# Performance work log

Hardware: AMD Instinct MI355X
Metric: run time of the kernel (lower is better)

Reference implementation:

```python
import jax, jax.numpy as jnp
import numpy as np

B, S, T, D = 64, 256, 8, 256
E, M = 500000, 2048
NEG_INF = -10000000000.0


def setup_inputs() -> dict:
    key = jax.random.key(0)
    ks = jax.random.split(key, 9)
    token_reprs = jax.random.normal(ks[0], (B, S, T, D), dtype=jnp.float32)
    w1 = jax.random.normal(ks[1], (D, D // 2), dtype=jnp.float32) * (1.0 / np.sqrt(D))
    b1 = jnp.zeros((D // 2,), dtype=jnp.float32)
    w2 = jax.random.normal(ks[2], (D // 2, 1), dtype=jnp.float32) * (1.0 / np.sqrt(D // 2))
    b2 = jnp.zeros((1,), dtype=jnp.float32)
    edge_index = jax.random.randint(ks[3], (2, E), 0, B * S, dtype=jnp.int32)
    lm_indices = jax.random.randint(ks[4], (M,), 0, B * S * T, dtype=jnp.int32)
    batch_pointers = jax.random.randint(ks[5], (M,), 0, B, dtype=jnp.int32)
    tree_padding_mask = jax.random.randint(ks[6], (B, S), 0, 2, dtype=jnp.int32).astype(jnp.bool_)
    return {
        "token_reprs": token_reprs,
        "w1": w1, "b1": b1, "w2": w2, "b2": b2,
        "edge_index": edge_index,
        "lm_indices": lm_indices,
        "batch_pointers": batch_pointers,
        "tree_padding_mask": tree_padding_mask,
    }


def reference(token_reprs, w1, b1, w2, b2, edge_index, lm_indices, batch_pointers, tree_padding_mask):
    b, s, t, d = token_reprs.shape
    # type representation is the first token of each type tree
    type_reprs = token_reprs[:, :, 0]                  # [B, S, D]
    flat_types = type_reprs.reshape(b * s, d)          # [B*S, D]

    # predict_lemmas: gather scope/goal reprs, elementwise multiply, 2-layer MLP
    scope_ids, goal_ids = edge_index[0], edge_index[1]
    h = flat_types[scope_ids] * flat_types[goal_ids]   # [E, D]
    h = h @ w1 + b1                                    # [E, D//2] (Dropout is identity in eval)
    lemmas = (h @ w2 + b2)[:, 0]                       # [E]

    # predict_masks: gather masked token reprs + per-tree candidates, dot, mask
    mask_reprs = token_reprs.reshape(b * s * t, d)[lm_indices]  # [M, D]
    candidates = type_reprs[batch_pointers]            # [M, S, D]
    candidate_mask = tree_padding_mask[batch_pointers] # [M, S]
    lm_preds = jnp.einsum('md,msd->ms', mask_reprs, candidates)
    lm_preds = jnp.where(candidate_mask, lm_preds, NEG_INF)
    return lemmas, lm_preds
```

## Files before the change

kernel.cpp:

```cpp
#include <hip/hip_runtime.h>

#define DD 256
#define SS 256
#define BB 64
#define NEDGE 500000
#define MM 2048
#define NEG_INF -10000000000.0f
#define ROWF4 512
#define NROWS (BB * SS)
#define EBLK 1954

#define OFF_VC     0
#define OFF_MSORT  2048
#define OFF_BSTART 10240
#define OFF_HIST   16384
#define OFF_EPAIR  (1 << 20)
#define OFF_EORIG  (6 << 20)
#define OFF_P2     (8 << 20)
#define OFF_QROW   (16 << 20)
#define OFF_MROWS  (24 << 20)

typedef _Float16 h2 __attribute__((ext_vector_type(2)));

__device__ __forceinline__ h2 uh(unsigned u) {
    union { unsigned x; h2 h; } c; c.x = u; return c.h;
}
__device__ __forceinline__ unsigned hpack(float a, float b) {
    union { h2 h; unsigned u; } c;
    c.h = h2{(_Float16)a, (_Float16)b};
    return c.u;
}

#if __has_builtin(__builtin_amdgcn_fdot2)
__device__ __forceinline__ float FDOT2(h2 a, h2 b, float c) {
    return __builtin_amdgcn_fdot2(a, b, c, false);
}
#else
__device__ __forceinline__ float FDOT2(h2 a, h2 b, float c) {
    return c + (float)a.x * (float)b.x + (float)a.y * (float)b.y;
}
#endif

__device__ __forceinline__ float dot16(uint4 a, uint4 b, float acc) {
    acc = FDOT2(uh(a.x), uh(b.x), acc);
    acc = FDOT2(uh(a.y), uh(b.y), acc);
    acc = FDOT2(uh(a.z), uh(b.z), acc);
    acc = FDOT2(uh(a.w), uh(b.w), acc);
    return acc;
}

__global__ void setup_k(const float* __restrict__ w1, const float* __restrict__ b1,
                        const float* __restrict__ w2, const float* __restrict__ b2,
                        const int* __restrict__ bp,
                        float* __restrict__ vc, int* __restrict__ msorted,
                        int* __restrict__ bstart, int* __restrict__ hist) {
    const int t = threadIdx.x;
    if (blockIdx.x == 0) {
        float acc = 0.f;
        #pragma unroll 4
        for (int j = 0; j < DD / 2; ++j) acc += w1[t * (DD / 2) + j] * w2[j];
        vc[t] = acc;
        if (t == 0) {
            float c = b2[0];
            for (int j = 0; j < DD / 2; ++j) c += b1[j] * w2[j];
            vc[DD] = c;
        }
    } else if (blockIdx.x == 1) {
        __shared__ int h[BB];
        __shared__ int offs[BB + 1];
        if (t < BB) h[t] = 0;
        __syncthreads();
        for (int m = t; m < MM; m += 256) atomicAdd(&h[bp[m]], 1);
        __syncthreads();
        if (t == 0) {
            int acc = 0;
            for (int i = 0; i < BB; ++i) { offs[i] = acc; acc += h[i]; }
            offs[BB] = acc;
        }
        __syncthreads();
        if (t < BB + 1) bstart[t] = offs[t];
        __syncthreads();
        for (int m = t; m < MM; m += 256) {
            int pos = atomicAdd(&offs[bp[m]], 1);
            msorted[pos] = m;
        }
    } else {
        for (int f = t; f < NROWS; f += 256) hist[f] = 0;
    }
}

__global__ __launch_bounds__(256) void compact_hist(
        const float* __restrict__ tok, const int* __restrict__ lmi,
        const int* __restrict__ edges, const float* __restrict__ vc,
        unsigned* __restrict__ p2u, unsigned* __restrict__ qrow,
        unsigned* __restrict__ mru, int* __restrict__ hist) {
    const int t = threadIdx.x;
    const int lane = t & 63, w = t >> 6;
    const int bid = blockIdx.x;
    if (bid < NROWS / 4) {
        const int row = bid * 4 + w;
        const float4 a = ((const float4*)tok)[(size_t)row * ROWF4 + lane];
        const float4 v = ((const float4*)vc)[lane];
        ((uint2*)p2u)[(size_t)row * 64 + lane] =
            make_uint2(hpack(a.x, a.y), hpack(a.z, a.w));
        ((uint2*)qrow)[(size_t)row * 64 + lane] =
            make_uint2(hpack(a.x * v.x, a.y * v.y), hpack(a.z * v.z, a.w * v.w));
    } else if (bid < NROWS / 4 + MM / 4) {
        const int m = (bid - NROWS / 4) * 4 + w;
        const float4 a = ((const float4*)(tok + (size_t)lmi[m] * DD))[lane];
        ((uint2*)mru)[(size_t)m * 64 + lane] =
            make_uint2(hpack(a.x, a.y), hpack(a.z, a.w));
    } else {
        const int e = (bid - NROWS / 4 - MM / 4) * 256 + t;
        if (e < NEDGE) atomicAdd(&hist[__builtin_nontemporal_load(edges + e)], 1);
    }
}

__global__ __launch_bounds__(256) void prefix_k(int* __restrict__ hist) {
    __shared__ int loc[NROWS];
    __shared__ int part[256];
    __shared__ int scan[256];
    const int t = threadIdx.x;
    for (int f = t; f < NROWS; f += 256) loc[f] = hist[f];
    __syncthreads();
    int s = 0;
    for (int j = 0; j < 64; ++j) s += loc[t * 64 + j];
    part[t] = s;
    __syncthreads();
    if (t == 0) {
        int a = 0;
        for (int i = 0; i < 256; ++i) { scan[i] = a; a += part[i]; }
    }
    __syncthreads();
    int a = scan[t];
    for (int j = 0; j < 64; ++j) {
        int c = loc[t * 64 + j];
        loc[t * 64 + j] = a;
        a += c;
    }
    __syncthreads();
    for (int f = t; f < NROWS; f += 256) hist[f] = loc[f];
}

__global__ __launch_bounds__(256) void scatter_k(
        const int* __restrict__ edges, int* __restrict__ hist,
        uint2* __restrict__ epair, unsigned* __restrict__ eorig) {
    const int e = blockIdx.x * 256 + threadIdx.x;
    if (e >= NEDGE) return;
    const int sc = __builtin_nontemporal_load(edges + e);
    const int gl = __builtin_nontemporal_load(edges + NEDGE + e);
    const int pos = atomicAdd(&hist[sc], 1);
    epair[pos] = make_uint2((unsigned)sc, (unsigned)gl);
    eorig[pos] = (unsigned)e;
}

__global__ __launch_bounds__(256) void edge_sorted(
        const unsigned* __restrict__ qrow, const unsigned* __restrict__ p2u,
        const uint2* __restrict__ epair, const unsigned* __restrict__ eorig,
        const float* __restrict__ vc, float* __restrict__ out) {
    const int t = threadIdx.x;
    const int l32 = t & 31, grp = t >> 5;
    __shared__ uint2 sPair[256];
    __shared__ unsigned sOrig[256];
    __shared__ float sRes[256];
    const int idx = blockIdx.x * 256 + t;
    const bool val = idx < NEDGE;
    sPair[t] = val ? epair[idx] : make_uint2(0u, 0u);
    sOrig[t] = val ? eorig[idx] : 0u;
    const float c = vc[DD];
    __syncthreads();

    const uint4* Q = (const uint4*)qrow;
    const uint4* A = (const uint4*)p2u;
    #pragma unroll 2
    for (int ii = 0; ii < 32; ++ii) {
        const int slot = grp * 32 + ii;
        const uint2 pr = sPair[slot];
        const uint4 qa = Q[(size_t)pr.x * 32 + l32];
        const uint4 ab = A[(size_t)pr.y * 32 + l32];
        float r = dot16(qa, ab, 0.f);
        r += __shfl_down(r, 16, 32);
        r += __shfl_down(r, 8, 32);
        r += __shfl_down(r, 4, 32);
        r += __shfl_down(r, 2, 32);
        r += __shfl_down(r, 1, 32);
        if (l32 == 0) sRes[slot] = r + c;
    }
    __syncthreads();
    if (val) __builtin_nontemporal_store(sRes[t], out + sOrig[t]);
}

__global__ __launch_bounds__(256) void lm_gemm(
        const unsigned* __restrict__ p2u,
        const unsigned* __restrict__ mru,
        const int* __restrict__ msorted,
        const int* __restrict__ bstart,
        const int* __restrict__ tpm,
        float* __restrict__ out) {
    const int b  = blockIdx.x;
    const int st = blockIdx.y;
    const int ch = blockIdx.z;
    const int s0 = bstart[b], nmt = bstart[b + 1] - s0;
    const int base = ch * 32;
    if (base >= nmt) return;
    const int nm = min(32, nmt - base);
    const int t = threadIdx.x;

    __shared__ uint4 candS[64 * 33];
    __shared__ uint4 maskS[32 * 33];
    __shared__ int mids[32];

    if (t < 32) mids[t] = msorted[s0 + base + min(t, nm - 1)];
    __syncthreads();
    for (int f = t; f < 32 * 32; f += 256) {
        const int r = f >> 5, q = f & 31;
        maskS[r * 33 + q] = ((const uint4*)mru)[(size_t)mids[r] * 32 + q];
    }
    for (int f = t; f < 64 * 32; f += 256) {
        const int r = f >> 5, q = f & 31;
        candS[r * 33 + q] = ((const uint4*)p2u)[((size_t)b * SS + st * 64 + r) * 32 + q];
    }
    __syncthreads();

    const int tmg = t & 15, tsg = t >> 4;
    float acc[2][4];
    #pragma unroll
    for (int im = 0; im < 2; ++im)
        #pragma unroll
        for (int ss = 0; ss < 4; ++ss) acc[im][ss] = 0.f;

    #pragma unroll 4
    for (int j = 0; j < 32; ++j) {
        const uint4 a0 = maskS[tmg * 33 + j];
        const uint4 a1 = maskS[(tmg + 16) * 33 + j];
        #pragma unroll
        for (int ss = 0; ss < 4; ++ss) {
            const uint4 bb = candS[(tsg * 4 + ss) * 33 + j];
            acc[0][ss] = dot16(a0, bb, acc[0][ss]);
            acc[1][ss] = dot16(a1, bb, acc[1][ss]);
        }
    }

    const int col0 = st * 64 + tsg * 4;
    float4 msk;
    msk.x = tpm[b * SS + col0] ? 1.f : 0.f;
    msk.y = tpm[b * SS + col0 + 1] ? 1.f : 0.f;
    msk.z = tpm[b * SS + col0 + 2] ? 1.f : 0.f;
    msk.w = tpm[b * SS + col0 + 3] ? 1.f : 0.f;
    #pragma unroll
    for (int im = 0; im < 2; ++im) {
        const int mi = tmg + im * 16;
        if (mi < nm) {
            float4 o;
            o.x = msk.x != 0.f ? acc[im][0] : NEG_INF;
            o.y = msk.y != 0.f ? acc[im][1] : NEG_INF;
            o.z = msk.z != 0.f ? acc[im][2] : NEG_INF;
            o.w = msk.w != 0.f ? acc[im][3] : NEG_INF;
            *(float4*)&out[(size_t)mids[mi] * SS + col0] = o;
        }
    }
}

extern "C" void kernel_launch(void* const* d_in, const int* in_sizes, int n_in,
                              void* d_out, int out_size, void* d_ws, size_t ws_size,
                              hipStream_t stream) {
    const float* tok = (const float*)d_in[0];
    const float* w1  = (const float*)d_in[1];
    const float* b1  = (const float*)d_in[2];
    const float* w2  = (const float*)d_in[3];
    const float* b2  = (const float*)d_in[4];
    const int* edges = (const int*)d_in[5];
    const int* lmi   = (const int*)d_in[6];
    const int* bp    = (const int*)d_in[7];
    const int* tpm   = (const int*)d_in[8];

    float* out_lemmas = (float*)d_out;
    float* out_lm     = (float*)d_out + NEDGE;

    char* ws = (char*)d_ws;
    float* vc       = (float*)(ws + OFF_VC);
    int* msorted    = (int*)(ws + OFF_MSORT);
    int* bstart     = (int*)(ws + OFF_BSTART);
    int* hist       = (int*)(ws + OFF_HIST);
    uint2* epair    = (uint2*)(ws + OFF_EPAIR);
    unsigned* eorig = (unsigned*)(ws + OFF_EORIG);
    unsigned* p2u   = (unsigned*)(ws + OFF_P2);
    unsigned* qrow  = (unsigned*)(ws + OFF_QROW);
    unsigned* mru   = (unsigned*)(ws + OFF_MROWS);

    setup_k<<<3, 256, 0, stream>>>(w1, b1, w2, b2, bp, vc, msorted, bstart, hist);
    compact_hist<<<NROWS / 4 + MM / 4 + EBLK, 256, 0, stream>>>(
        tok, lmi, edges, vc, p2u, qrow, mru, hist);
    prefix_k<<<1, 256, 0, stream>>>(hist);
    scatter_k<<<EBLK, 256, 0, stream>>>(edges, hist, epair, eorig);
    edge_sorted<<<EBLK, 256, 0, stream>>>(qrow, p2u, epair, eorig, vc, out_lemmas);
    lm_gemm<<<dim3(BB, 4, 4), 256, 0, stream>>>(p2u, mru, msorted, bstart, tpm, out_lm);
}
```

Baseline: 297.4 us.

## Bucket edges by scope/goal row ranges and pin buckets to XCDs

Replaces the full counting sort of edges by scope row (16K-bin histogram plus a single-block prefix scan) with a coarse 64-bucket sort keyed on the high bits of scope and goal ids. Each block builds a shared-memory histogram first, which cuts global atomics. The edge kernel now launches 512 persistent blocks, each handling an eighth of its assigned buckets, with blockIdx mod 8 steering its bucket sequence so each XCD's L2 works on one row range at a time. It writes results directly to out[eorig] and drops the staged shared-memory gather. The trade-off is a looser scope ordering, uncoalesced scattered stores, and load imbalance within a bucket.

```diff
diff --git a/kernel.cpp b/kernel.cpp
--- a/kernel.cpp
+++ b/kernel.cpp
@@ -13,7 +13,8 @@
 #define OFF_VC     0
 #define OFF_MSORT  2048
 #define OFF_BSTART 10240
-#define OFF_HIST   16384
+#define OFF_EBKT   11264
+#define OFF_CURS   12288
 #define OFF_EPAIR  (1 << 20)
 #define OFF_EORIG  (6 << 20)
 #define OFF_P2     (8 << 20)
@@ -53,7 +54,8 @@
                         const float* __restrict__ w2, const float* __restrict__ b2,
                         const int* __restrict__ bp,
                         float* __restrict__ vc, int* __restrict__ msorted,
-                        int* __restrict__ bstart, int* __restrict__ hist) {
+                        int* __restrict__ bstart, int* __restrict__ ebkt,
+                        int* __restrict__ cursor) {
     const int t = threadIdx.x;
     if (blockIdx.x == 0) {
         float acc = 0.f;
@@ -85,7 +87,8 @@
             msorted[pos] = m;
         }
     } else {
-        for (int f = t; f < NROWS; f += 256) hist[f] = 0;
+        if (t < 65) ebkt[t] = 0;
+        if (t < 64) cursor[t] = 0;
     }
 }
 
@@ -93,7 +96,7 @@
         const float* __restrict__ tok, const int* __restrict__ lmi,
         const int* __restrict__ edges, const float* __restrict__ vc,
         unsigned* __restrict__ p2u, unsigned* __restrict__ qrow,
-        unsigned* __restrict__ mru, int* __restrict__ hist) {
+        unsigned* __restrict__ mru, int* __restrict__ ebkt) {
     const int t = threadIdx.x;
     const int lane = t & 63, w = t >> 6;
     const int bid = blockIdx.x;
@@ -111,83 +114,94 @@
         ((uint2*)mru)[(size_t)m * 64 + lane] =
             make_uint2(hpack(a.x, a.y), hpack(a.z, a.w));
     } else {
+        __shared__ int lh[64];
+        if (t < 64) lh[t] = 0;
+        __syncthreads();
         const int e = (bid - NROWS / 4 - MM / 4) * 256 + t;
-        if (e < NEDGE) atomicAdd(&hist[__builtin_nontemporal_load(edges + e)], 1);
-    }
-}
-
-__global__ __launch_bounds__(256) void prefix_k(int* __restrict__ hist) {
-    __shared__ int loc[NROWS];
-    __shared__ int part[256];
-    __shared__ int scan[256];
-    const int t = threadIdx.x;
-    for (int f = t; f < NROWS; f += 256) loc[f] = hist[f];
-    __syncthreads();
-    int s = 0;
-    for (int j = 0; j < 64; ++j) s += loc[t * 64 + j];
-    part[t] = s;
-    __syncthreads();
-    if (t == 0) {
-        int a = 0;
-        for (int i = 0; i < 256; ++i) { scan[i] = a; a += part[i]; }
-    }
-    __syncthreads();
-    int a = scan[t];
-    for (int j = 0; j < 64; ++j) {
-        int c = loc[t * 64 + j];
-        loc[t * 64 + j] = a;
-        a += c;
-    }
-    __syncthreads();
-    for (int f = t; f < NROWS; f += 256) hist[f] = loc[f];
+        if (e < NEDGE) {
+            const int sc = __builtin_nontemporal_load(edges + e);
+            const int gl = __builtin_nontemporal_load(edges + NEDGE + e);
+            atomicAdd(&lh[(sc >> 11) * 8 + (gl >> 11)], 1);
+        }
+        __syncthreads();
+        if (t < 64 && lh[t]) atomicAdd(&ebkt[t], lh[t]);
+    }
+}
+
+__global__ void prefix64(int* __restrict__ ebkt, int* __restrict__ cursor) {
+    if (threadIdx.x == 0) {
+        int acc = 0;
+        for (int i = 0; i < 64; ++i) {
+            int c = ebkt[i];
+            ebkt[i] = acc; cursor[i] = acc;
+            acc += c;
+        }
+        ebkt[64] = acc;
+    }
 }
 
 __global__ __launch_bounds__(256) void scatter_k(
-        const int* __restrict__ edges, int* __restrict__ hist,
+        const int* __restrict__ edges, int* __restrict__ cursor,
         uint2* __restrict__ epair, unsigned* __restrict__ eorig) {
-    const int e = blockIdx.x * 256 + threadIdx.x;
-    if (e >= NEDGE) return;
-    const int sc = __builtin_nontemporal_load(edges + e);
-    const int gl = __builtin_nontemporal_load(edges + NEDGE + e);
-    const int pos = atomicAdd(&hist[sc], 1);
-    epair[pos] = make_uint2((unsigned)sc, (unsigned)gl);
-    eorig[pos] = (unsigned)e;
-}
-
-__global__ __launch_bounds__(256) void edge_sorted(
+    __shared__ int lh[64], lbase[64], lcur[64];
+    const int t = threadIdx.x;
+    if (t < 64) lh[t] = 0;
+    __syncthreads();
+    const int e = blockIdx.x * 256 + t;
+    int sc = 0, gl = 0, bkt = 0;
+    const bool v = e < NEDGE;
+    if (v) {
+        sc = __builtin_nontemporal_load(edges + e);
+        gl = __builtin_nontemporal_load(edges + NEDGE + e);
+        bkt = (sc >> 11) * 8 + (gl >> 11);
+        atomicAdd(&lh[bkt], 1);
+    }
+    __syncthreads();
+    if (t < 64) {
+        lbase[t] = lh[t] ? atomicAdd(&cursor[t], lh[t]) : 0;
+        lcur[t] = 0;
+    }
+    __syncthreads();
+    if (v) {
+        const int r = atomicAdd(&lcur[bkt], 1);
+        const int pos = lbase[bkt] + r;
+        epair[pos] = make_uint2((unsigned)sc, (unsigned)gl);
+        eorig[pos] = (unsigned)e;
+    }
+}
+
+__global__ __launch_bounds__(256) void edge_xcd(
         const unsigned* __restrict__ qrow, const unsigned* __restrict__ p2u,
         const uint2* __restrict__ epair, const unsigned* __restrict__ eorig,
-        const float* __restrict__ vc, float* __restrict__ out) {
+        const int* __restrict__ ebkt, const float* __restrict__ vc,
+        float* __restrict__ out) {
     const int t = threadIdx.x;
     const int l32 = t & 31, grp = t >> 5;
-    __shared__ uint2 sPair[256];
-    __shared__ unsigned sOrig[256];
-    __shared__ float sRes[256];
-    const int idx = blockIdx.x * 256 + t;
-    const bool val = idx < NEDGE;
-    sPair[t] = val ? epair[idx] : make_uint2(0u, 0u);
-    sOrig[t] = val ? eorig[idx] : 0u;
+    const int g = blockIdx.x & 7;
+    const int w = blockIdx.x >> 3;
     const float c = vc[DD];
-    __syncthreads();
-
     const uint4* Q = (const uint4*)qrow;
     const uint4* A = (const uint4*)p2u;
-    #pragma unroll 2
-    for (int ii = 0; ii < 32; ++ii) {
-        const int slot = grp * 32 + ii;
-        const uint2 pr = sPair[slot];
-        const uint4 qa = Q[(size_t)pr.x * 32 + l32];
-        const uint4 ab = A[(size_t)pr.y * 32 + l32];
-        float r = dot16(qa, ab, 0.f);
-        r += __shfl_down(r, 16, 32);
-        r += __shfl_down(r, 8, 32);
-        r += __shfl_down(r, 4, 32);
-        r += __shfl_down(r, 2, 32);
-        r += __shfl_down(r, 1, 32);
-        if (l32 == 0) sRes[slot] = r + c;
-    }
-    __syncthreads();
-    if (val) __builtin_nontemporal_store(sRes[t], out + sOrig[t]);
+    #pragma unroll 1
+    for (int p = 0; p < 8; ++p) {
+        const int bkt = p * 8 + ((p + g) & 7);
+        const int S = ebkt[bkt];
+        const int L = ebkt[bkt + 1] - S;
+        const int lo = S + (L * w >> 6);
+        const int hi = S + (L * (w + 1) >> 6);
+        for (int i = lo + grp; i < hi; i += 8) {
+            const uint2 pr = epair[i];
+            const uint4 qa = Q[(size_t)pr.x * 32 + l32];
+            const uint4 ab = A[(size_t)pr.y * 32 + l32];
+            float r = dot16(qa, ab, 0.f);
+            r += __shfl_down(r, 16, 32);
+            r += __shfl_down(r, 8, 32);
+            r += __shfl_down(r, 4, 32);
+            r += __shfl_down(r, 2, 32);
+            r += __shfl_down(r, 1, 32);
+            if (l32 == 0) out[eorig[i]] = r + c;
+        }
+    }
 }
 
 __global__ __launch_bounds__(256) void lm_gemm(
@@ -281,18 +295,20 @@
     float* vc       = (float*)(ws + OFF_VC);
     int* msorted    = (int*)(ws + OFF_MSORT);
     int* bstart     = (int*)(ws + OFF_BSTART);
-    int* hist       = (int*)(ws + OFF_HIST);
+    int* ebkt       = (int*)(ws + OFF_EBKT);
+    int* cursor     = (int*)(ws + OFF_CURS);
     uint2* epair    = (uint2*)(ws + OFF_EPAIR);
     unsigned* eorig = (unsigned*)(ws + OFF_EORIG);
     unsigned* p2u   = (unsigned*)(ws + OFF_P2);
     unsigned* qrow  = (unsigned*)(ws + OFF_QROW);
     unsigned* mru   = (unsigned*)(ws + OFF_MROWS);
 
-    setup_k<<<3, 256, 0, stream>>>(w1, b1, w2, b2, bp, vc, msorted, bstart, hist);
+    setup_k<<<3, 256, 0, stream>>>(w1, b1, w2, b2, bp, vc, msorted, bstart,
+                                   ebkt, cursor);
     compact_hist<<<NROWS / 4 + MM / 4 + EBLK, 256, 0, stream>>>(
-        tok, lmi, edges, vc, p2u, qrow, mru, hist);
-    prefix_k<<<1, 256, 0, stream>>>(hist);
-    scatter_k<<<EBLK, 256, 0, stream>>>(edges, hist, epair, eorig);
-    edge_sorted<<<EBLK, 256, 0, stream>>>(qrow, p2u, epair, eorig, vc, out_lemmas);
+        tok, lmi, edges, vc, p2u, qrow, mru, ebkt);
+    prefix64<<<1, 64, 0, stream>>>(ebkt, cursor);
+    scatter_k<<<EBLK, 256, 0, stream>>>(edges, cursor, epair, eorig);
+    edge_xcd<<<512, 256, 0, stream>>>(qrow, p2u, epair, eorig, ebkt, vc, out_lemmas);
     lm_gemm<<<dim3(BB, 4, 4), 256, 0, stream>>>(p2u, mru, msorted, bstart, tpm, out_lm);
 }
```

After: 389.7 us. 1.31x slower.
